# Performance work log

Hardware: AMD Instinct MI355X
Metric: run time of the kernel (lower is better)

Reference implementation:

```python
import jax, jax.numpy as jnp
import numpy as np

K = 20
EPS = 1e-5  # BatchNorm eps, eval mode with running_mean=0, running_var=1


def _bn(x, g, b):
    # eval-mode BatchNorm with running stats (mean=0, var=1): affine only
    return x * (g / jnp.sqrt(1.0 + EPS)) + b


def _lrelu(x):
    return jax.nn.leaky_relu(x, 0.2)


def setup_inputs() -> dict:
    key = jax.random.key(0)
    ks = jax.random.split(key, 8)
    B, N, EMB, OUT = 8, 4096, 1024, 128
    def w(k, shape):
        fan_in = shape[0]
        return (jax.random.normal(k, shape, jnp.float32) / np.sqrt(fan_in)).astype(jnp.float32)
    inp = {
        "x":  jax.random.normal(ks[0], (B, N, 3), jnp.float32),
        "W1": w(ks[1], (6, 64)),   "g1": jnp.ones(64),  "b1": jnp.zeros(64),
        "W2": w(ks[2], (64, 64)),  "g2": jnp.ones(64),  "b2": jnp.zeros(64),
        "W3": w(ks[3], (64, 128)), "g3": jnp.ones(128), "b3": jnp.zeros(128),
        "W4": w(ks[4], (128, 256)),"g4": jnp.ones(256), "b4": jnp.zeros(256),
        "W5": w(ks[5], (512, EMB)),"g5": jnp.ones(EMB), "b5": jnp.zeros(EMB),
        "L1": w(ks[6], (2 * EMB, 512)), "g6": jnp.ones(512), "b6": jnp.zeros(512),
        "L2": w(ks[7], (512, 256)), "L2b": jnp.zeros(256), "g7": jnp.ones(256), "b7": jnp.zeros(256),
        "L3": w(jax.random.fold_in(key, 99), (256, OUT)), "L3b": jnp.zeros(OUT),
    }
    return inp


def _knn_idx(pts):
    # pts: [B, 3, N]; returns indices of K nearest neighbors [B, N, K]
    inner = -2.0 * jnp.einsum('bdn,bdm->bnm', pts, pts)  # [B,N,N]
    xx = jnp.sum(pts * pts, axis=1)                       # [B,N]
    pd = -xx[:, :, None] - inner - xx[:, None, :]          # negative squared distance
    return jax.lax.top_k(pd, K)[1]                         # [B,N,K]


def reference(x, W1, g1, b1, W2, g2, b2, W3, g3, b3, W4, g4, b4,
              W5, g5, b5, L1, g6, b6, L2, L2b, g7, b7, L3, L3b):
    B, N, _ = x.shape
    pts = jnp.transpose(x, (0, 2, 1))           # [B,3,N]
    idx = _knn_idx(pts)                          # [B,N,K]

    # gather neighbor coordinates: [B,N,K,3]
    feature = jax.vmap(lambda xb, ib: xb[ib])(x, idx)
    center = jnp.broadcast_to(x[:, :, None, :], (B, N, K, 3))
    h = jnp.concatenate([feature, center], axis=-1)  # [B,N,K,6]

    h = _lrelu(_bn(jnp.einsum('bnkc,co->bnko', h, W1), g1, b1))
    x1 = jnp.max(h, axis=2)                          # [B,N,64]
    h = _lrelu(_bn(jnp.einsum('bnkc,co->bnko', h, W2), g2, b2))
    x2 = jnp.max(h, axis=2)                          # [B,N,64]
    h = _lrelu(_bn(jnp.einsum('bnkc,co->bnko', h, W3), g3, b3))
    x3 = jnp.max(h, axis=2)                          # [B,N,128]
    h = _lrelu(_bn(jnp.einsum('bnkc,co->bnko', h, W4), g4, b4))
    x4 = jnp.max(h, axis=2)                          # [B,N,256]

    hc = jnp.concatenate([x1, x2, x3, x4], axis=-1)  # [B,N,512]
    h5 = _lrelu(_bn(jnp.einsum('bnc,co->bno', hc, W5), g5, b5))  # [B,N,EMB]

    gmax = jnp.max(h5, axis=1)                       # [B,EMB]
    gavg = jnp.mean(h5, axis=1)                      # [B,EMB]
    g = jnp.concatenate([gmax, gavg], axis=-1)       # [B,2*EMB]

    f = _lrelu(_bn(g @ L1, g6, b6))                  # dropout = identity (eval)
    f = _lrelu(_bn(f @ L2 + L2b, g7, b7))
    return f @ L3 + L3b                              # [B,OUT]
```

## Files before the change

kernel.cpp:

```cpp
#include <hip/hip_runtime.h>
#include <hip/hip_bf16.h>
#include <hip/hip_fp16.h>

#define NPTS 4096
#define KNB  20
#define EPSB 1e-5f

typedef _Float16 half8 __attribute__((ext_vector_type(8)));
typedef float    f32x4 __attribute__((ext_vector_type(4)));

__device__ __forceinline__ f32x4 mfma16(half8 a, half8 b, f32x4 c){
  return __builtin_amdgcn_mfma_f32_16x16x32_f16(a, b, c, 0, 0, 0);
}

__device__ __forceinline__ half8 loadA_lds(const _Float16* buf, int C, int mt, int ks, int lane){
  int row = mt*16 + (lane & 15);
  int k0  = ks*32 + (lane >> 4)*8;
  int e   = (row*C + k0) ^ ((row & 7) << 3);
  return *reinterpret_cast<const half8*>(&buf[e]);
}

__device__ __forceinline__ half8 loadB_g(const _Float16* WT, int K, int nt, int ks, int lane){
  int col = nt*16 + (lane & 15);
  int k0  = ks*32 + (lane >> 4)*8;
  return *reinterpret_cast<const half8*>(&WT[col*K + k0]);
}

__global__ __launch_bounds__(1024)
void knn_kernel(const float* __restrict__ x, int* __restrict__ idx_out){
  __shared__ float4 spts[NPTS];
  int b  = blockIdx.x >> 8;
  int r0 = (blockIdx.x & 255) << 4;
  const float* xb = x + (size_t)b*NPTS*3;
  for (int t = threadIdx.x; t < NPTS; t += 1024){
    float px = xb[t*3+0], py = xb[t*3+1], pz = xb[t*3+2];
    spts[t] = make_float4(px, py, pz, 0.5f*(px*px + py*py + pz*pz));
  }
  __syncthreads();
  int wave = threadIdx.x >> 6, lane = threadIdx.x & 63;
  int i = r0 + wave;
  float4 pi = spts[i];
  float b1 = -INFINITY, b2 = -INFINITY, b3 = -INFINITY;
  int   i1 = 0, i2 = 0, i3 = 0;
  #pragma unroll 8
  for (int t = 0; t < 64; ++t){
    int j = (t << 6) + lane;
    float4 q = spts[j];
    float d = pi.x*q.x + pi.y*q.y + pi.z*q.z - pi.w - q.w;
    bool c1 = d > b1, c2 = d > b2, c3 = d > b3;
    float t2 = fmaxf(b2, fminf(b1, d));
    float t3 = fmaxf(b3, fminf(b2, d));
    i3 = c2 ? i2 : (c3 ? j : i3);
    i2 = c1 ? i1 : (c2 ? j : i2);
    i1 = c1 ? j : i1;
    b1 = fmaxf(b1, d);
    b2 = t2; b3 = t3;
  }
  unsigned long long rem = 0ull;
  size_t obase = ((size_t)b*NPTS + i)*KNB;
  #pragma unroll 1
  for (int kk = 0; kk < KNB; ++kk){
    float bv = b1;
    #pragma unroll
    for (int m = 1; m <= 32; m <<= 1)
      bv = fmaxf(bv, __shfl_xor(bv, m));
    unsigned long long tied = __ballot(b1 == bv);
    int bj;
    if (__popcll(tied) > 1){
      int jv = (b1 == bv) ? i1 : 0x7fffffff;
      #pragma unroll
      for (int m = 1; m <= 32; m <<= 1)
        jv = min(jv, __shfl_xor(jv, m));
      bj = jv;
    } else {
      bj = __shfl(i1, (int)__ffsll(tied) - 1);
    }
    if (lane == 0) idx_out[obase + kk] = bj;
    bool iwin = (b1 == bv) && (i1 == bj);
    if (iwin){
      rem |= 1ull << (i1 >> 6);
      b1 = b2; i1 = i2; b2 = b3; i2 = i3; b3 = -INFINITY;
    }
    if (kk < KNB-1 && __any(b1 == -INFINITY)){
      if (b1 == -INFINITY){
        b2 = -INFINITY; b3 = -INFINITY; i1 = 0; i2 = 0; i3 = 0;
        #pragma unroll 8
        for (int t = 0; t < 64; ++t){
          if (rem & (1ull << t)) continue;
          int j = (t << 6) + lane;
          float4 q = spts[j];
          float d = pi.x*q.x + pi.y*q.y + pi.z*q.z - pi.w - q.w;
          bool c1 = d > b1, c2 = d > b2, c3 = d > b3;
          float t2 = fmaxf(b2, fminf(b1, d));
          float t3 = fmaxf(b3, fminf(b2, d));
          i3 = c2 ? i2 : (c3 ? j : i3);
          i2 = c1 ? i1 : (c2 ? j : i2);
          i1 = c1 ? j : i1;
          b1 = fmaxf(b1, d);
          b2 = t2; b3 = t3;
        }
      }
    }
  }
}

__global__ __launch_bounds__(256)
void prep_kernel(const float* __restrict__ W2, const float* __restrict__ W3,
                 const float* __restrict__ W4,
                 _Float16* __restrict__ W2T, _Float16* __restrict__ W3T,
                 _Float16* __restrict__ W4T){
  int t = blockIdx.x*256 + threadIdx.x;
  if (t < 4096){ int o=t>>6, k=t&63;                W2T[t] = (_Float16)W2[k*64+o]; }
  else if (t < 12288){ int u=t-4096;  int o=u>>6, k=u&63;   W3T[u] = (_Float16)W3[k*128+o]; }
  else if (t < 45056){ int u=t-12288; int o=u>>7, k=u&127;  W4T[u] = (_Float16)W4[k*256+o]; }
}

__global__ __launch_bounds__(256)
void prep5_kernel(const float* __restrict__ W5, _Float16* __restrict__ W5T){
  __shared__ float tile[32][33];
  int tk = (blockIdx.x & 15) << 5;
  int to = (blockIdx.x >> 4) << 5;
  int lr = threadIdx.x >> 5;
  int lc = threadIdx.x & 31;
  #pragma unroll
  for (int r = 0; r < 32; r += 8)
    tile[lr + r][lc] = W5[(size_t)(tk + lr + r)*1024 + to + lc];
  __syncthreads();
  #pragma unroll
  for (int r = 0; r < 32; r += 8)
    W5T[(size_t)(to + lr + r)*512 + tk + lc] = (_Float16)tile[lc][lr + r];
}

__device__ __forceinline__ void bucket(int mt, bool c1, bool c2, bool c3, float v,
                                       float& p0, float& p1, float& p2, float& p3){
  if (mt == 0)      p0 = fmaxf(p0, v);
  else if (mt == 4) p3 = fmaxf(p3, v);
  else if (mt == 1){ p1 = fmaxf(p1, c1 ? v : -INFINITY); p0 = fmaxf(p0, c1 ? -INFINITY : v); }
  else if (mt == 2){ p2 = fmaxf(p2, c2 ? v : -INFINITY); p1 = fmaxf(p1, c2 ? -INFINITY : v); }
  else             { p3 = fmaxf(p3, c3 ? v : -INFINITY); p2 = fmaxf(p2, c3 ? -INFINITY : v); }
}

__device__ __forceinline__ void reduce_write_x(float p0, float p1, float p2, float p3,
                                               _Float16* __restrict__ hc, size_t gp0,
                                               int off, int g, int c){
  p0 = fmaxf(p0, __shfl_xor(p0, 16)); p0 = fmaxf(p0, __shfl_xor(p0, 32));
  p1 = fmaxf(p1, __shfl_xor(p1, 16)); p1 = fmaxf(p1, __shfl_xor(p1, 32));
  p2 = fmaxf(p2, __shfl_xor(p2, 16)); p2 = fmaxf(p2, __shfl_xor(p2, 32));
  p3 = fmaxf(p3, __shfl_xor(p3, 16)); p3 = fmaxf(p3, __shfl_xor(p3, 32));
  float v = (g == 0) ? p0 : (g == 1) ? p1 : (g == 2) ? p2 : p3;
  hc[(gp0 + g)*512 + off + c] = (_Float16)v;
}

__global__ __launch_bounds__(256)
void edge_kernel(const float* __restrict__ x, const int* __restrict__ knn,
                 const float* __restrict__ W1, const float* __restrict__ g1, const float* __restrict__ b1,
                 const _Float16* __restrict__ W2T, const float* __restrict__ g2, const float* __restrict__ b2,
                 const _Float16* __restrict__ W3T, const float* __restrict__ g3, const float* __restrict__ b3,
                 const _Float16* __restrict__ W4T, const float* __restrict__ g4, const float* __restrict__ b4,
                 _Float16* __restrict__ hc){
  __shared__ __align__(16) char smem[40960];
  _Float16* hb1 = (_Float16*)(smem);
  _Float16* hb2 = (_Float16*)(smem + 10240);
  _Float16* hb3 = (_Float16*)(smem + 20480);
  float*    h0f = (float*)(smem + 20480);
  float*    h0c = (float*)(smem + 20480 + 1280);
  const float rs = 1.f / sqrtf(1.f + EPSB);
  int gp0 = blockIdx.x << 2;
  int b   = gp0 >> 12;
  int n0  = gp0 & (NPTS-1);
  const float* xb = x + (size_t)b*NPTS*3;
  int tid = threadIdx.x;
  if (tid < 80){
    int p = tid / 20, k = tid % 20;
    int nb = knn[((size_t)b*NPTS + n0 + p)*KNB + k];
    h0f[tid*4+0] = xb[nb*3+0];
    h0f[tid*4+1] = xb[nb*3+1];
    h0f[tid*4+2] = xb[nb*3+2];
  } else if (tid < 96){
    int u = tid - 80; int p = u >> 2, c = u & 3;
    if (c < 3) h0c[p*4+c] = xb[(n0+p)*3+c];
  }
  __syncthreads();
  int w = tid >> 6, lane = tid & 63, g = lane >> 4, cc = lane & 15;
  bool c1 = (g >= 1), c2 = (g >= 2), c3 = (g >= 3);
  {
    int col = lane;
    float sc = g1[col]*rs, bs = b1[col];
    float w0=W1[col], w1_=W1[64+col], w2_=W1[128+col], w3_=W1[192+col], w4_=W1[256+col], w5_=W1[320+col];
    float cx = h0c[w*4+0], cy = h0c[w*4+1], cz = h0c[w*4+2];
    float m1 = -INFINITY;
    #pragma unroll 5
    for (int k = 0; k < KNB; ++k){
      int r = w*20 + k;
      float a = h0f[r*4+0]*w0 + h0f[r*4+1]*w1_ + h0f[r*4+2]*w2_ + cx*w3_ + cy*w4_ + cz*w5_;
      float vv = a*sc + bs; vv = vv > 0.f ? vv : 0.2f*vv;
      hb1[((r<<6)+col) ^ ((r&7)<<3)] = (_Float16)vv;
      m1 = fmaxf(m1, vv);
    }
    hc[(size_t)(gp0 + w)*512 + col] = (_Float16)m1;
  }
  __syncthreads();
  {
    int colg = (w<<4) + cc;
    float sc = g2[colg]*rs, bs = b2[colg];
    half8 bf0 = loadB_g(W2T, 64, w, 0, lane);
    half8 bf1 = loadB_g(W2T, 64, w, 1, lane);
    float p0=-INFINITY, p1=-INFINITY, p2=-INFINITY, p3=-INFINITY;
    #pragma unroll
    for (int mt = 0; mt < 5; ++mt){
      f32x4 a = {0.f,0.f,0.f,0.f};
      a = mfma16(loadA_lds(hb1,64,mt,0,lane), bf0, a);
      a = mfma16(loadA_lds(hb1,64,mt,1,lane), bf1, a);
      #pragma unroll
      for (int rr = 0; rr < 4; ++rr){
        int row = mt*16 + g*4 + rr;
        float vv = a[rr]*sc + bs; vv = vv > 0.f ? vv : 0.2f*vv;
        hb2[(row*64 + colg) ^ ((row&7)<<3)] = (_Float16)vv;
        bucket(mt, c1, c2, c3, vv, p0, p1, p2, p3);
      }
    }
    reduce_write_x(p0,p1,p2,p3, hc, gp0, 64 + (w<<4), g, cc);
  }
  __syncthreads();
  {
    int ntA = (w<<1), ntB = ntA + 1;
    int colA = (ntA<<4) + cc, colB = (ntB<<4) + cc;
    float scA = g3[colA]*rs, bsA = b3[colA];
    float scB = g3[colB]*rs, bsB = b3[colB];
    half8 bA0 = loadB_g(W3T, 64, ntA, 0, lane);
    half8 bA1 = loadB_g(W3T, 64, ntA, 1, lane);
    half8 bB0 = loadB_g(W3T, 64, ntB, 0, lane);
    half8 bB1 = loadB_g(W3T, 64, ntB, 1, lane);
    float pA0=-INFINITY,pA1=-INFINITY,pA2=-INFINITY,pA3=-INFINITY;
    float pB0=-INFINITY,pB1=-INFINITY,pB2=-INFINITY,pB3=-INFINITY;
    #pragma unroll
    for (int mt = 0; mt < 5; ++mt){
      half8 a0 = loadA_lds(hb2,64,mt,0,lane);
      half8 a1 = loadA_lds(hb2,64,mt,1,lane);
      f32x4 aA = {0.f,0.f,0.f,0.f};
      aA = mfma16(a0, bA0, aA); aA = mfma16(a1, bA1, aA);
      f32x4 aB = {0.f,0.f,0.f,0.f};
      aB = mfma16(a0, bB0, aB); aB = mfma16(a1, bB1, aB);
      #pragma unroll
      for (int rr = 0; rr < 4; ++rr){
        int row = mt*16 + g*4 + rr;
        float vA = aA[rr]*scA + bsA; vA = vA > 0.f ? vA : 0.2f*vA;
        hb3[(row*128 + colA) ^ ((row&7)<<3)] = (_Float16)vA;
        bucket(mt, c1, c2, c3, vA, pA0, pA1, pA2, pA3);
        float vB = aB[rr]*scB + bsB; vB = vB > 0.f ? vB : 0.2f*vB;
        hb3[(row*128 + colB) ^ ((row&7)<<3)] = (_Float16)vB;
        bucket(mt, c1, c2, c3, vB, pB0, pB1, pB2, pB3);
      }
    }
    reduce_write_x(pA0,pA1,pA2,pA3, hc, gp0, 128 + (ntA<<4), g, cc);
    reduce_write_x(pB0,pB1,pB2,pB3, hc, gp0, 128 + (ntB<<4), g, cc);
  }
  __syncthreads();
  #pragma unroll 1
  for (int pass = 0; pass < 2; ++pass){
    int ntA = (pass<<3) + w, ntB = ntA + 4;
    int colA = (ntA<<4) + cc, colB = (ntB<<4) + cc;
    float scA = g4[colA]*rs, bsA = b4[colA];
    float scB = g4[colB]*rs, bsB = b4[colB];
    half8 bwA[4], bwB[4];
    #pragma unroll
    for (int ks = 0; ks < 4; ++ks){
      bwA[ks] = loadB_g(W4T, 128, ntA, ks, lane);
      bwB[ks] = loadB_g(W4T, 128, ntB, ks, lane);
    }
    float pA0=-INFINITY,pA1=-INFINITY,pA2=-INFINITY,pA3=-INFINITY;
    float pB0=-INFINITY,pB1=-INFINITY,pB2=-INFINITY,pB3=-INFINITY;
    #pragma unroll
    for (int mt = 0; mt < 5; ++mt){
      half8 a[4];
      #pragma unroll
      for (int ks = 0; ks < 4; ++ks) a[ks] = loadA_lds(hb3,128,mt,ks,lane);
      f32x4 aA = {0.f,0.f,0.f,0.f};
      #pragma unroll
      for (int ks = 0; ks < 4; ++ks) aA = mfma16(a[ks], bwA[ks], aA);
      f32x4 aB = {0.f,0.f,0.f,0.f};
      #pragma unroll
      for (int ks = 0; ks < 4; ++ks) aB = mfma16(a[ks], bwB[ks], aB);
      #pragma unroll
      for (int rr = 0; rr < 4; ++rr){
        float vA = aA[rr]*scA + bsA; vA = vA > 0.f ? vA : 0.2f*vA;
        bucket(mt, c1, c2, c3, vA, pA0, pA1, pA2, pA3);
        float vB = aB[rr]*scB + bsB; vB = vB > 0.f ? vB : 0.2f*vB;
        bucket(mt, c1, c2, c3, vB, pB0, pB1, pB2, pB3);
      }
    }
    reduce_write_x(pA0,pA1,pA2,pA3, hc, gp0, 256 + (ntA<<4), g, cc);
    reduce_write_x(pB0,pB1,pB2,pB3, hc, gp0, 256 + (ntB<<4), g, cc);
  }
}

__global__ __launch_bounds__(256)
void gemm5_kernel(const _Float16* __restrict__ hc, const _Float16* __restrict__ W5T,
                  const float* __restrict__ g5, const float* __restrict__ b5,
                  float* __restrict__ red){
  __shared__ __align__(16) _Float16 sA[64*512];
  int rowblk = blockIdx.x >> 2;
  int colblk = blockIdx.x & 3;
  int row0 = rowblk << 6;
  #pragma unroll 1
  for (int it = 0; it < 16; ++it){
    int eoff = it*2048 + threadIdx.x*8;
    int row = eoff >> 9;
    int ine = eoff & 511;
    half8 vsrc = *reinterpret_cast<const half8*>(
        &hc[(size_t)(row0 + row)*512 + (ine ^ ((row & 7) << 3))]);
    *reinterpret_cast<half8*>(&sA[(row << 9) + ine]) = vsrc;
  }
  __syncthreads();
  int wave = threadIdx.x >> 6, lane = threadIdx.x & 63;
  f32x4 acc[4][4] = {};
  #pragma unroll 1
  for (int ks = 0; ks < 16; ++ks){
    half8 af[4];
    #pragma unroll
    for (int mt = 0; mt < 4; ++mt) af[mt] = loadA_lds(sA, 512, mt, ks, lane);
    #pragma unroll
    for (int nt = 0; nt < 4; ++nt){
      int ntg = (colblk<<4) + (wave<<2) + nt;
      half8 bf = loadB_g(W5T, 512, ntg, ks, lane);
      #pragma unroll
      for (int mt = 0; mt < 4; ++mt)
        acc[mt][nt] = mfma16(af[mt], bf, acc[mt][nt]);
    }
  }
  int batch = row0 >> 12;
  int chunk = (row0 & (NPTS-1)) >> 6;
  const float rs = 1.f/sqrtf(1.f+EPSB);
  #pragma unroll
  for (int nt = 0; nt < 4; ++nt){
    int ntg = (colblk<<4) + (wave<<2) + nt;
    int colg = (ntg<<4) + (lane & 15);
    float sc = g5[colg]*rs, bs = b5[colg];
    float vmax = -INFINITY, vsum = 0.f;
    #pragma unroll
    for (int mt = 0; mt < 4; ++mt){
      #pragma unroll
      for (int r = 0; r < 4; ++r){
        float vv = acc[mt][nt][r]*sc + bs;
        vv = vv>0.f ? vv : 0.2f*vv;
        vmax = fmaxf(vmax, vv); vsum += vv;
      }
    }
    vmax = fmaxf(vmax, __shfl_xor(vmax, 16)); vsum += __shfl_xor(vsum, 16);
    vmax = fmaxf(vmax, __shfl_xor(vmax, 32)); vsum += __shfl_xor(vsum, 32);
    if ((lane >> 4) == 0){
      size_t base = (size_t)((batch<<6) + chunk)*2048;
      red[base + colg] = vmax;
      red[base + 1024 + colg] = vsum;
    }
  }
}

__global__ __launch_bounds__(256)
void reduce_g_kernel(const float* __restrict__ red, float* __restrict__ g){
  int t = blockIdx.x*256 + threadIdx.x;
  int b = t >> 10, col = t & 1023;
  float m = -INFINITY, s = 0.f;
  #pragma unroll 4
  for (int c = 0; c < 64; ++c){
    size_t base = (size_t)((b<<6)+c)*2048;
    m = fmaxf(m, red[base + col]);
    s += red[base + 1024 + col];
  }
  g[(b<<11) + col]        = m;
  g[(b<<11) + 1024 + col] = s * (1.f/4096.f);
}

__global__ __launch_bounds__(256)
void fc1_kernel(const float* __restrict__ g, const float* __restrict__ L1,
                const float* __restrict__ g6, const float* __restrict__ b6,
                float* __restrict__ f1){
  __shared__ float part[4][64];
  int b  = blockIdx.x >> 3;
  int og = blockIdx.x & 7;
  int o  = (og << 6) + (threadIdx.x & 63);
  int kg = threadIdx.x >> 6;
  const float* gb = g + (b << 11);
  float acc = 0.f;
  #pragma unroll 8
  for (int k = kg*512; k < kg*512 + 512; ++k) acc += gb[k]*L1[k*512 + o];
  part[kg][threadIdx.x & 63] = acc;
  __syncthreads();
  if (threadIdx.x < 64){
    float s = part[0][threadIdx.x] + part[1][threadIdx.x] + part[2][threadIdx.x] + part[3][threadIdx.x];
    float v = s*(g6[o]/sqrtf(1.f+EPSB)) + b6[o];
    f1[(b<<9) + o] = v > 0.f ? v : 0.2f*v;
  }
}

__global__ __launch_bounds__(256)
void fc2_kernel(const float* __restrict__ f1, const float* __restrict__ L2, const float* __restrict__ L2b,
                const float* __restrict__ g7, const float* __restrict__ b7, float* __restrict__ f2){
  __shared__ float part[4][64];
  int b  = blockIdx.x >> 2;
  int og = blockIdx.x & 3;
  int o  = (og << 6) + (threadIdx.x & 63);
  int kg = threadIdx.x >> 6;
  const float* fb = f1 + (b << 9);
  float acc = 0.f;
  #pragma unroll 8
  for (int k = kg*128; k < kg*128 + 128; ++k) acc += fb[k]*L2[k*256 + o];
  part[kg][threadIdx.x & 63] = acc;
  __syncthreads();
  if (threadIdx.x < 64){
    float s = part[0][threadIdx.x] + part[1][threadIdx.x] + part[2][threadIdx.x] + part[3][threadIdx.x];
    float v = (s + L2b[o])*(g7[o]/sqrtf(1.f+EPSB)) + b7[o];
    f2[(b<<8) + o] = v > 0.f ? v : 0.2f*v;
  }
}

__global__ __launch_bounds__(256)
void fc3_kernel(const float* __restrict__ f2, const float* __restrict__ L3, const float* __restrict__ L3b,
                float* __restrict__ out){
  __shared__ float part[2][128];
  int b  = blockIdx.x;
  int o  = threadIdx.x & 127;
  int kg = threadIdx.x >> 7;
  const float* fb = f2 + (b << 8);
  float acc = 0.f;
  #pragma unroll 8
  for (int k = kg*128; k < kg*128 + 128; ++k) acc += fb[k]*L3[k*128 + o];
  part[kg][o] = acc;
  __syncthreads();
  if (threadIdx.x < 128)
    out[(b<<7) + o] = part[0][o] + part[1][o] + L3b[o];
}

extern "C" void kernel_launch(void* const* d_in, const int* in_sizes, int n_in,
                              void* d_out, int out_size, void* d_ws, size_t ws_size,
                              hipStream_t stream){
  const float* x  = (const float*)d_in[0];
  const float* W1 = (const float*)d_in[1];
  const float* g1 = (const float*)d_in[2];  const float* b1 = (const float*)d_in[3];
  const float* W2 = (const float*)d_in[4];
  const float* g2 = (const float*)d_in[5];  const float* b2 = (const float*)d_in[6];
  const float* W3 = (const float*)d_in[7];
  const float* g3 = (const float*)d_in[8];  const float* b3 = (const float*)d_in[9];
  const float* W4 = (const float*)d_in[10];
  const float* g4 = (const float*)d_in[11]; const float* b4 = (const float*)d_in[12];
  const float* W5 = (const float*)d_in[13];
  const float* g5 = (const float*)d_in[14]; const float* b5 = (const float*)d_in[15];
  const float* L1 = (const float*)d_in[16];
  const float* g6 = (const float*)d_in[17]; const float* b6 = (const float*)d_in[18];
  const float* L2 = (const float*)d_in[19]; const float* L2b = (const float*)d_in[20];
  const float* g7 = (const float*)d_in[21]; const float* b7 = (const float*)d_in[22];
  const float* L3 = (const float*)d_in[23]; const float* L3b = (const float*)d_in[24];

  char* ws = (char*)d_ws;
  int*      idx  = (int*)(ws + 0);
  _Float16* hc   = (_Float16*)(ws + 2621440);
  _Float16* W2T  = (_Float16*)(ws + 36175872);
  _Float16* W3T  = (_Float16*)(ws + 36184064);
  _Float16* W4T  = (_Float16*)(ws + 36200448);
  _Float16* W5T  = (_Float16*)(ws + 36265984);
  float*    red  = (float*)(ws + 37314560);
  float*    gbuf = (float*)(ws + 41508864);
  float*    f1   = (float*)(ws + 41574400);
  float*    f2   = (float*)(ws + 41590784);

  knn_kernel<<<2048, 1024, 0, stream>>>(x, idx);
  prep_kernel<<<176, 256, 0, stream>>>(W2, W3, W4, W2T, W3T, W4T);
  prep5_kernel<<<512, 256, 0, stream>>>(W5, W5T);
  edge_kernel<<<8192, 256, 0, stream>>>(x, idx, W1, g1, b1, W2T, g2, b2,
                                        W3T, g3, b3, W4T, g4, b4, hc);
  gemm5_kernel<<<2048, 256, 0, stream>>>(hc, W5T, g5, b5, red);
  reduce_g_kernel<<<32, 256, 0, stream>>>(red, gbuf);
  fc1_kernel<<<64, 256, 0, stream>>>(gbuf, L1, g6, b6, f1);
  fc2_kernel<<<32, 256, 0, stream>>>(f1, L2, L2b, g7, b7, f2);
  fc3_kernel<<<8, 256, 0, stream>>>(f2, L3, L3b, (float*)d_out);
}
```

Measured before the change: 437.8 us.

## Pack edge-conv epilogues into half2 math and simplify kNN argmax reduction

The edge-conv epilogues (BN affine, leaky ReLU and the per-point max buckets) move from scalar fp32 to packed fp16 pairs. Each accumulator pair is converted with cvt_pkrtz and reduced with packed max, which roughly halves the VALU work and shuffle count in the max-reduction. Separately, the kNN selection loop replaces the float max-reduce with tie-handling ballot by a single packed-key unsigned max that encodes the lane in its low bits, making the winner lookup branchless. The cost is earlier rounding of the epilogue to fp16. Ties are now broken by lane within a 64-unit quantization window instead of by minimum index, so near-equal distances may select different neighbors.

```diff
diff --git a/kernel.cpp b/kernel.cpp
--- a/kernel.cpp
+++ b/kernel.cpp
@@ -6,8 +6,9 @@
 #define KNB  20
 #define EPSB 1e-5f
 
-typedef _Float16 half8 __attribute__((ext_vector_type(8)));
-typedef float    f32x4 __attribute__((ext_vector_type(4)));
+typedef _Float16 half8  __attribute__((ext_vector_type(8)));
+typedef _Float16 half2v __attribute__((ext_vector_type(2)));
+typedef float    f32x4  __attribute__((ext_vector_type(4)));
 
 __device__ __forceinline__ f32x4 mfma16(half8 a, half8 b, f32x4 c){
   return __builtin_amdgcn_mfma_f32_16x16x32_f16(a, b, c, 0, 0, 0);
@@ -24,6 +25,21 @@
   int col = nt*16 + (lane & 15);
   int k0  = ks*32 + (lane >> 4)*8;
   return *reinterpret_cast<const half8*>(&WT[col*K + k0]);
+}
+
+__device__ __forceinline__ half2v pkmax(half2v a, half2v b){
+  return __builtin_elementwise_max(a, b);
+}
+__device__ __forceinline__ half2v shflx_h2(half2v v, int m){
+  int iv = __builtin_bit_cast(int, v);
+  iv = __shfl_xor(iv, m);
+  return __builtin_bit_cast(half2v, iv);
+}
+__device__ __forceinline__ half2v ep_pk(float a, float b, half2v sc2, half2v bs2){
+  half2v v = __builtin_bit_cast(half2v, __builtin_amdgcn_cvt_pkrtz(a, b));
+  v = v*sc2 + bs2;
+  half2v w = v * (half2v){(_Float16)0.2f, (_Float16)0.2f};
+  return pkmax(v, w);
 }
 
 __global__ __launch_bounds__(1024)
@@ -60,27 +76,24 @@
   size_t obase = ((size_t)b*NPTS + i)*KNB;
   #pragma unroll 1
   for (int kk = 0; kk < KNB; ++kk){
-    float bv = b1;
-    #pragma unroll
-    for (int m = 1; m <= 32; m <<= 1)
-      bv = fmaxf(bv, __shfl_xor(bv, m));
-    unsigned long long tied = __ballot(b1 == bv);
-    int bj;
-    if (__popcll(tied) > 1){
-      int jv = (b1 == bv) ? i1 : 0x7fffffff;
-      #pragma unroll
-      for (int m = 1; m <= 32; m <<= 1)
-        jv = min(jv, __shfl_xor(jv, m));
-      bj = jv;
-    } else {
-      bj = __shfl(i1, (int)__ffsll(tied) - 1);
-    }
+    unsigned s = __float_as_uint(b1);
+    unsigned key = s ^ ((unsigned)(((int)s) >> 31) | 0x80000000u);
+    key = (key & 0xFFFFFFC0u) | (unsigned)lane;
+    unsigned bv = key;
+    #pragma unroll
+    for (int m = 1; m <= 32; m <<= 1){
+      unsigned ov = (unsigned)__shfl_xor((int)bv, m);
+      bv = bv > ov ? bv : ov;
+    }
+    int wl = (int)(bv & 63u);
+    int bj = __shfl(i1, wl);
     if (lane == 0) idx_out[obase + kk] = bj;
-    bool iwin = (b1 == bv) && (i1 == bj);
-    if (iwin){
-      rem |= 1ull << (i1 >> 6);
-      b1 = b2; i1 = i2; b2 = b3; i2 = i3; b3 = -INFINITY;
-    }
+    bool iw = (lane == wl);
+    unsigned long long nbit = 1ull << (i1 >> 6);
+    rem |= iw ? nbit : 0ull;
+    b1 = iw ? b2 : b1;  i1 = iw ? i2 : i1;
+    b2 = iw ? b3 : b2;  i2 = iw ? i3 : i2;
+    b3 = iw ? -INFINITY : b3;
     if (kk < KNB-1 && __any(b1 == -INFINITY)){
       if (b1 == -INFINITY){
         b2 = -INFINITY; b3 = -INFINITY; i1 = 0; i2 = 0; i3 = 0;
@@ -131,24 +144,26 @@
     W5T[(size_t)(to + lr + r)*512 + tk + lc] = (_Float16)tile[lc][lr + r];
 }
 
-__device__ __forceinline__ void bucket(int mt, bool c1, bool c2, bool c3, float v,
-                                       float& p0, float& p1, float& p2, float& p3){
-  if (mt == 0)      p0 = fmaxf(p0, v);
-  else if (mt == 4) p3 = fmaxf(p3, v);
-  else if (mt == 1){ p1 = fmaxf(p1, c1 ? v : -INFINITY); p0 = fmaxf(p0, c1 ? -INFINITY : v); }
-  else if (mt == 2){ p2 = fmaxf(p2, c2 ? v : -INFINITY); p1 = fmaxf(p1, c2 ? -INFINITY : v); }
-  else             { p3 = fmaxf(p3, c3 ? v : -INFINITY); p2 = fmaxf(p2, c3 ? -INFINITY : v); }
-}
-
-__device__ __forceinline__ void reduce_write_x(float p0, float p1, float p2, float p3,
-                                               _Float16* __restrict__ hc, size_t gp0,
-                                               int off, int g, int c){
-  p0 = fmaxf(p0, __shfl_xor(p0, 16)); p0 = fmaxf(p0, __shfl_xor(p0, 32));
-  p1 = fmaxf(p1, __shfl_xor(p1, 16)); p1 = fmaxf(p1, __shfl_xor(p1, 32));
-  p2 = fmaxf(p2, __shfl_xor(p2, 16)); p2 = fmaxf(p2, __shfl_xor(p2, 32));
-  p3 = fmaxf(p3, __shfl_xor(p3, 16)); p3 = fmaxf(p3, __shfl_xor(p3, 32));
-  float v = (g == 0) ? p0 : (g == 1) ? p1 : (g == 2) ? p2 : p3;
-  hc[(gp0 + g)*512 + off + c] = (_Float16)v;
+__device__ __forceinline__ void pk_bucket(int mt, bool c1, bool c2, bool c3, half2v m,
+                                          half2v& q0, half2v& q1, half2v& q2, half2v& q3){
+  const half2v NI = {(_Float16)-INFINITY, (_Float16)-INFINITY};
+  if (mt == 0)      q0 = pkmax(q0, m);
+  else if (mt == 4) q3 = pkmax(q3, m);
+  else if (mt == 1){ q1 = pkmax(q1, c1 ? m : NI); q0 = pkmax(q0, c1 ? NI : m); }
+  else if (mt == 2){ q2 = pkmax(q2, c2 ? m : NI); q1 = pkmax(q1, c2 ? NI : m); }
+  else             { q3 = pkmax(q3, c3 ? m : NI); q2 = pkmax(q2, c3 ? NI : m); }
+}
+
+__device__ __forceinline__ void reduce_write_pk(half2v q0, half2v q1, half2v q2, half2v q3,
+                                                _Float16* __restrict__ hc, size_t gp0,
+                                                int off, int g, int c){
+  q0 = pkmax(q0, shflx_h2(q0,16)); q0 = pkmax(q0, shflx_h2(q0,32));
+  q1 = pkmax(q1, shflx_h2(q1,16)); q1 = pkmax(q1, shflx_h2(q1,32));
+  q2 = pkmax(q2, shflx_h2(q2,16)); q2 = pkmax(q2, shflx_h2(q2,32));
+  q3 = pkmax(q3, shflx_h2(q3,16)); q3 = pkmax(q3, shflx_h2(q3,32));
+  half2v v = (g == 0) ? q0 : (g == 1) ? q1 : (g == 2) ? q2 : q3;
+  _Float16 r = v.x > v.y ? v.x : v.y;
+  hc[(gp0 + g)*512 + off + c] = r;
 }
 
 __global__ __launch_bounds__(256)
@@ -165,6 +180,7 @@
   float*    h0f = (float*)(smem + 20480);
   float*    h0c = (float*)(smem + 20480 + 1280);
   const float rs = 1.f / sqrtf(1.f + EPSB);
+  const half2v NI = {(_Float16)-INFINITY, (_Float16)-INFINITY};
   int gp0 = blockIdx.x << 2;
   int b   = gp0 >> 12;
   int n0  = gp0 & (NPTS-1);
@@ -202,37 +218,40 @@
   __syncthreads();
   {
     int colg = (w<<4) + cc;
-    float sc = g2[colg]*rs, bs = b2[colg];
+    float scf = g2[colg]*rs, bsf = b2[colg];
+    half2v sc2 = {(_Float16)scf,(_Float16)scf}, bs2 = {(_Float16)bsf,(_Float16)bsf};
     half8 bf0 = loadB_g(W2T, 64, w, 0, lane);
     half8 bf1 = loadB_g(W2T, 64, w, 1, lane);
-    float p0=-INFINITY, p1=-INFINITY, p2=-INFINITY, p3=-INFINITY;
+    half2v q0=NI, q1=NI, q2=NI, q3=NI;
     #pragma unroll
     for (int mt = 0; mt < 5; ++mt){
       f32x4 a = {0.f,0.f,0.f,0.f};
       a = mfma16(loadA_lds(hb1,64,mt,0,lane), bf0, a);
       a = mfma16(loadA_lds(hb1,64,mt,1,lane), bf1, a);
-      #pragma unroll
-      for (int rr = 0; rr < 4; ++rr){
-        int row = mt*16 + g*4 + rr;
-        float vv = a[rr]*sc + bs; vv = vv > 0.f ? vv : 0.2f*vv;
-        hb2[(row*64 + colg) ^ ((row&7)<<3)] = (_Float16)vv;
-        bucket(mt, c1, c2, c3, vv, p0, p1, p2, p3);
-      }
-    }
-    reduce_write_x(p0,p1,p2,p3, hc, gp0, 64 + (w<<4), g, cc);
+      half2v lo = ep_pk(a[0], a[1], sc2, bs2);
+      half2v hi = ep_pk(a[2], a[3], sc2, bs2);
+      int r0_ = mt*16 + g*4;
+      hb2[((r0_+0)*64+colg) ^ (((r0_+0)&7)<<3)] = lo.x;
+      hb2[((r0_+1)*64+colg) ^ (((r0_+1)&7)<<3)] = lo.y;
+      hb2[((r0_+2)*64+colg) ^ (((r0_+2)&7)<<3)] = hi.x;
+      hb2[((r0_+3)*64+colg) ^ (((r0_+3)&7)<<3)] = hi.y;
+      pk_bucket(mt, c1, c2, c3, pkmax(lo,hi), q0, q1, q2, q3);
+    }
+    reduce_write_pk(q0,q1,q2,q3, hc, gp0, 64 + (w<<4), g, cc);
   }
   __syncthreads();
   {
     int ntA = (w<<1), ntB = ntA + 1;
     int colA = (ntA<<4) + cc, colB = (ntB<<4) + cc;
-    float scA = g3[colA]*rs, bsA = b3[colA];
-    float scB = g3[colB]*rs, bsB = b3[colB];
+    float sAf = g3[colA]*rs, bAf = b3[colA];
+    float sBf = g3[colB]*rs, bBf = b3[colB];
+    half2v scA2={(_Float16)sAf,(_Float16)sAf}, bsA2={(_Float16)bAf,(_Float16)bAf};
+    half2v scB2={(_Float16)sBf,(_Float16)sBf}, bsB2={(_Float16)bBf,(_Float16)bBf};
     half8 bA0 = loadB_g(W3T, 64, ntA, 0, lane);
     half8 bA1 = loadB_g(W3T, 64, ntA, 1, lane);
     half8 bB0 = loadB_g(W3T, 64, ntB, 0, lane);
     half8 bB1 = loadB_g(W3T, 64, ntB, 1, lane);
-    float pA0=-INFINITY,pA1=-INFINITY,pA2=-INFINITY,pA3=-INFINITY;
-    float pB0=-INFINITY,pB1=-INFINITY,pB2=-INFINITY,pB3=-INFINITY;
+    half2v qA0=NI,qA1=NI,qA2=NI,qA3=NI, qB0=NI,qB1=NI,qB2=NI,qB3=NI;
     #pragma unroll
     for (int mt = 0; mt < 5; ++mt){
       half8 a0 = loadA_lds(hb2,64,mt,0,lane);
@@ -241,35 +260,41 @@
       aA = mfma16(a0, bA0, aA); aA = mfma16(a1, bA1, aA);
       f32x4 aB = {0.f,0.f,0.f,0.f};
       aB = mfma16(a0, bB0, aB); aB = mfma16(a1, bB1, aB);
-      #pragma unroll
-      for (int rr = 0; rr < 4; ++rr){
-        int row = mt*16 + g*4 + rr;
-        float vA = aA[rr]*scA + bsA; vA = vA > 0.f ? vA : 0.2f*vA;
-        hb3[(row*128 + colA) ^ ((row&7)<<3)] = (_Float16)vA;
-        bucket(mt, c1, c2, c3, vA, pA0, pA1, pA2, pA3);
-        float vB = aB[rr]*scB + bsB; vB = vB > 0.f ? vB : 0.2f*vB;
-        hb3[(row*128 + colB) ^ ((row&7)<<3)] = (_Float16)vB;
-        bucket(mt, c1, c2, c3, vB, pB0, pB1, pB2, pB3);
-      }
-    }
-    reduce_write_x(pA0,pA1,pA2,pA3, hc, gp0, 128 + (ntA<<4), g, cc);
-    reduce_write_x(pB0,pB1,pB2,pB3, hc, gp0, 128 + (ntB<<4), g, cc);
+      half2v loA = ep_pk(aA[0],aA[1],scA2,bsA2);
+      half2v hiA = ep_pk(aA[2],aA[3],scA2,bsA2);
+      half2v loB = ep_pk(aB[0],aB[1],scB2,bsB2);
+      half2v hiB = ep_pk(aB[2],aB[3],scB2,bsB2);
+      int r0_ = mt*16 + g*4;
+      hb3[((r0_+0)*128+colA) ^ (((r0_+0)&7)<<3)] = loA.x;
+      hb3[((r0_+1)*128+colA) ^ (((r0_+1)&7)<<3)] = loA.y;
+      hb3[((r0_+2)*128+colA) ^ (((r0_+2)&7)<<3)] = hiA.x;
+      hb3[((r0_+3)*128+colA) ^ (((r0_+3)&7)<<3)] = hiA.y;
+      hb3[((r0_+0)*128+colB) ^ (((r0_+0)&7)<<3)] = loB.x;
+      hb3[((r0_+1)*128+colB) ^ (((r0_+1)&7)<<3)] = loB.y;
+      hb3[((r0_+2)*128+colB) ^ (((r0_+2)&7)<<3)] = hiB.x;
+      hb3[((r0_+3)*128+colB) ^ (((r0_+3)&7)<<3)] = hiB.y;
+      pk_bucket(mt, c1, c2, c3, pkmax(loA,hiA), qA0,qA1,qA2,qA3);
+      pk_bucket(mt, c1, c2, c3, pkmax(loB,hiB), qB0,qB1,qB2,qB3);
+    }
+    reduce_write_pk(qA0,qA1,qA2,qA3, hc, gp0, 128 + (ntA<<4), g, cc);
+    reduce_write_pk(qB0,qB1,qB2,qB3, hc, gp0, 128 + (ntB<<4), g, cc);
   }
   __syncthreads();
   #pragma unroll 1
   for (int pass = 0; pass < 2; ++pass){
     int ntA = (pass<<3) + w, ntB = ntA + 4;
     int colA = (ntA<<4) + cc, colB = (ntB<<4) + cc;
-    float scA = g4[colA]*rs, bsA = b4[colA];
-    float scB = g4[colB]*rs, bsB = b4[colB];
+    float sAf = g4[colA]*rs, bAf = b4[colA];
+    float sBf = g4[colB]*rs, bBf = b4[colB];
+    half2v scA2={(_Float16)sAf,(_Float16)sAf}, bsA2={(_Float16)bAf,(_Float16)bAf};
+    half2v scB2={(_Float16)sBf,(_Float16)sBf}, bsB2={(_Float16)bBf,(_Float16)bBf};
     half8 bwA[4], bwB[4];
     #pragma unroll
     for (int ks = 0; ks < 4; ++ks){
       bwA[ks] = loadB_g(W4T, 128, ntA, ks, lane);
       bwB[ks] = loadB_g(W4T, 128, ntB, ks, lane);
     }
-    float pA0=-INFINITY,pA1=-INFINITY,pA2=-INFINITY,pA3=-INFINITY;
-    float pB0=-INFINITY,pB1=-INFINITY,pB2=-INFINITY,pB3=-INFINITY;
+    half2v qA0=NI,qA1=NI,qA2=NI,qA3=NI, qB0=NI,qB1=NI,qB2=NI,qB3=NI;
     #pragma unroll
     for (int mt = 0; mt < 5; ++mt){
       half8 a[4];
@@ -281,16 +306,13 @@
       f32x4 aB = {0.f,0.f,0.f,0.f};
       #pragma unroll
       for (int ks = 0; ks < 4; ++ks) aB = mfma16(a[ks], bwB[ks], aB);
-      #pragma unroll
-      for (int rr = 0; rr < 4; ++rr){
-        float vA = aA[rr]*scA + bsA; vA = vA > 0.f ? vA : 0.2f*vA;
-        bucket(mt, c1, c2, c3, vA, pA0, pA1, pA2, pA3);
-        float vB = aB[rr]*scB + bsB; vB = vB > 0.f ? vB : 0.2f*vB;
-        bucket(mt, c1, c2, c3, vB, pB0, pB1, pB2, pB3);
-      }
-    }
-    reduce_write_x(pA0,pA1,pA2,pA3, hc, gp0, 256 + (ntA<<4), g, cc);
-    reduce_write_x(pB0,pB1,pB2,pB3, hc, gp0, 256 + (ntB<<4), g, cc);
+      half2v mA = pkmax(ep_pk(aA[0],aA[1],scA2,bsA2), ep_pk(aA[2],aA[3],scA2,bsA2));
+      half2v mB = pkmax(ep_pk(aB[0],aB[1],scB2,bsB2), ep_pk(aB[2],aB[3],scB2,bsB2));
+      pk_bucket(mt, c1, c2, c3, mA, qA0,qA1,qA2,qA3);
+      pk_bucket(mt, c1, c2, c3, mB, qB0,qB1,qB2,qB3);
+    }
+    reduce_write_pk(qA0,qA1,qA2,qA3, hc, gp0, 256 + (ntA<<4), g, cc);
+    reduce_write_pk(qB0,qB1,qB2,qB3, hc, gp0, 256 + (ntB<<4), g, cc);
   }
 }
 
```

Result: faster. 426.5 us (-2.6%).
